# Optimization experiments

Measured on AMD Instinct MI355X. Metric: run time of the kernel, lower is better.

## Reference

```python
import jax, jax.numpy as jnp
import numpy as np

NUM_ENTITIES = 102400
NUM_RELATIONS = 1000
EMB_DIM = 256
BATCH = 512
CHUNK = 1024  # entity-table tile size; keeps the [B, CHUNK, D] diff block ~512MB


def _xavier_row_normalized(key, shape):
    # nn.init.xavier_uniform_ followed by F.normalize(p=2, dim=1)
    bound = float(np.sqrt(6.0 / (shape[0] + shape[1])))
    w = jax.random.uniform(key, shape, jnp.float32, -bound, bound)
    return w / jnp.linalg.norm(w, axis=1, keepdims=True)


def setup_inputs() -> dict:
    key = jax.random.key(0)
    k1, k2, k3, k4 = jax.random.split(key, 4)
    entity_emb = _xavier_row_normalized(k1, (NUM_ENTITIES, EMB_DIM))
    relation_emb = _xavier_row_normalized(k2, (NUM_RELATIONS, EMB_DIM))
    h_idx = jax.random.randint(k3, (BATCH,), 0, NUM_ENTITIES, dtype=jnp.int32)
    r_idx = jax.random.randint(k4, (BATCH,), 0, NUM_RELATIONS, dtype=jnp.int32)
    return {"entity_emb": entity_emb, "relation_emb": relation_emb,
            "h_idx": h_idx, "r_idx": r_idx}


def _l1_cdist(x, table, chunk=CHUNK):
    # Tiled L1 pairwise distance: avoids materializing [B, N, D].
    B, D = x.shape
    nb = table.shape[0] // chunk
    blocks = table.reshape(nb, chunk, D)

    def body(tb):  # tb: [chunk, D] -> [B, chunk]
        return jnp.sum(jnp.abs(x[:, None, :] - tb[None, :, :]), axis=-1)

    d = jax.lax.map(body, blocks)                 # [nb, B, chunk]
    return jnp.transpose(d, (1, 0, 2)).reshape(B, nb * chunk)


def reference(entity_emb, relation_emb, h_idx, r_idx):
    # TransE.score_all_tails: -cdist(h + r, all_entities, p=1)
    x = entity_emb[h_idx] + relation_emb[r_idx]   # [B, D]
    return -_l1_cdist(x, entity_emb)              # [B, NUM_ENTITIES]
```

## Files before the change

kernel.cpp:

```cpp
#include <hip/hip_runtime.h>
#include <stdint.h>

#define NE 102400
#define DIM 256
#define NB 512
#define KROW (DIM / 4)

#define BM 256
#define BN 128
#define DT 128
#define KT (DT / 4)

#define SQ 384.0f
#define NINV (-1.0f / 384.0f)

#define XQ_BYTES ((size_t)NB * KROW * 4)
#define EQ_BYTES ((size_t)NE * KROW * 4)

typedef float vf4 __attribute__((ext_vector_type(4)));

static __device__ __forceinline__ uint32_t quant4(float a, float b, float c,
                                                  float d) {
  uint32_t q = 0;
  asm("v_cvt_pk_u8_f32 %0, %1, 0, %0" : "+v"(q) : "v"(fmaf(a, SQ, 128.5f)));
  asm("v_cvt_pk_u8_f32 %0, %1, 1, %0" : "+v"(q) : "v"(fmaf(b, SQ, 128.5f)));
  asm("v_cvt_pk_u8_f32 %0, %1, 2, %0" : "+v"(q) : "v"(fmaf(c, SQ, 128.5f)));
  asm("v_cvt_pk_u8_f32 %0, %1, 3, %0" : "+v"(q) : "v"(fmaf(d, SQ, 128.5f)));
  return q;
}

__global__ __launch_bounds__(64) void make_xq_kernel(
    const float* __restrict__ ent, const float* __restrict__ rel,
    const int* __restrict__ h_idx, const int* __restrict__ r_idx,
    uint32_t* __restrict__ xq) {
  const int b = blockIdx.x;
  const int t = threadIdx.x;
  const float4 e = *(const float4*)&ent[(size_t)h_idx[b] * DIM + t * 4];
  const float4 r = *(const float4*)&rel[(size_t)r_idx[b] * DIM + t * 4];
  xq[(size_t)b * KROW + t] = quant4(e.x + r.x, e.y + r.y, e.z + r.z, e.w + r.w);
}

__global__ __launch_bounds__(256) void quant_ent_kernel(
    const float* __restrict__ ent, uint32_t* __restrict__ eq) {
  const int n = blockIdx.x * 4 + (threadIdx.x >> 6);
  const int t = threadIdx.x & 63;
  const float4 v = *(const float4*)&ent[(size_t)n * DIM + t * 4];
  eq[(size_t)n * KROW + t] = quant4(v.x, v.y, v.z, v.w);
}

__global__ __launch_bounds__(256, 2) void transe_sad_q_kernel(
    const uint32_t* __restrict__ eq, const uint32_t* __restrict__ xq,
    float* __restrict__ out) {
  __shared__ uint32_t xT[KT][BM];
  __shared__ uint32_t eT[KT][BN];

  const int n0 = blockIdx.x * BN;
  const int b0 = blockIdx.y * BM;
  const int tid = threadIdx.x;
  const int tx = tid & 15;
  const int ty = tid >> 4;
  const int s_row = tid >> 1;
  const int s_half = tid & 1;

  uint32_t acc[16][8];
#pragma unroll
  for (int i = 0; i < 16; ++i)
#pragma unroll
    for (int j = 0; j < 8; ++j) acc[i][j] = 0u;

  for (int d0 = 0; d0 < DIM; d0 += DT) {
    {
      const uint4* src = (const uint4*)&xq[(size_t)(b0 + tid) * KROW + d0 / 4];
#pragma unroll
      for (int q = 0; q < 8; ++q) {
        uint4 v = src[q];
        xT[q * 4 + 0][tid] = v.x;
        xT[q * 4 + 1][tid] = v.y;
        xT[q * 4 + 2][tid] = v.z;
        xT[q * 4 + 3][tid] = v.w;
      }
    }
    {
      const uint4* src =
          (const uint4*)&eq[(size_t)(n0 + s_row) * KROW + d0 / 4 + s_half * 16];
#pragma unroll
      for (int q = 0; q < 4; ++q) {
        uint4 v = src[q];
        const int k = s_half * 16 + q * 4;
        eT[k + 0][s_row] = v.x;
        eT[k + 1][s_row] = v.y;
        eT[k + 2][s_row] = v.z;
        eT[k + 3][s_row] = v.w;
      }
    }
    __syncthreads();

#pragma unroll 2
    for (int k = 0; k < KT; ++k) {
      uint32_t xw[16], ew[8];
      *(uint4*)&xw[0]  = *(const uint4*)&xT[k][ty * 4];
      *(uint4*)&xw[4]  = *(const uint4*)&xT[k][64 + ty * 4];
      *(uint4*)&xw[8]  = *(const uint4*)&xT[k][128 + ty * 4];
      *(uint4*)&xw[12] = *(const uint4*)&xT[k][192 + ty * 4];
      *(uint4*)&ew[0]  = *(const uint4*)&eT[k][tx * 4];
      *(uint4*)&ew[4]  = *(const uint4*)&eT[k][64 + tx * 4];
#pragma unroll
      for (int i = 0; i < 16; ++i)
#pragma unroll
        for (int j = 0; j < 8; ++j)
          asm("v_sad_u8 %0, %1, %2, %0"
              : "+v"(acc[i][j])
              : "v"(xw[i]), "v"(ew[j]));
    }
    __syncthreads();
  }

#pragma unroll
  for (int i = 0; i < 16; ++i) {
    const int b = b0 + (i >> 2) * 64 + ty * 4 + (i & 3);
    float* dst = &out[(size_t)b * NE + n0];
    vf4 o0, o1;
    o0.x = (float)acc[i][0] * NINV;
    o0.y = (float)acc[i][1] * NINV;
    o0.z = (float)acc[i][2] * NINV;
    o0.w = (float)acc[i][3] * NINV;
    o1.x = (float)acc[i][4] * NINV;
    o1.y = (float)acc[i][5] * NINV;
    o1.z = (float)acc[i][6] * NINV;
    o1.w = (float)acc[i][7] * NINV;
    __builtin_nontemporal_store(o0, (vf4*)&dst[tx * 4]);
    __builtin_nontemporal_store(o1, (vf4*)&dst[64 + tx * 4]);
  }
}

__global__ __launch_bounds__(256) void transe_sad_f32_kernel(
    const float* __restrict__ ent, const uint32_t* __restrict__ xq,
    float* __restrict__ out) {
  __shared__ uint32_t xT[KT][128];
  __shared__ uint32_t eT[KT][BN];

  const int n0 = blockIdx.x * BN;
  const int b0 = blockIdx.y * 128;
  const int tid = threadIdx.x;
  const int tx = tid & 15;
  const int ty = tid >> 4;
  const int s_row = tid >> 1;
  const int s_half = tid & 1;

  uint32_t acc[8][8];
#pragma unroll
  for (int i = 0; i < 8; ++i)
#pragma unroll
    for (int j = 0; j < 8; ++j) acc[i][j] = 0u;

  for (int d0 = 0; d0 < DIM; d0 += DT) {
    {
      const uint4* src =
          (const uint4*)&xq[(size_t)(b0 + s_row) * KROW + d0 / 4 + s_half * 16];
#pragma unroll
      for (int q = 0; q < 4; ++q) {
        uint4 v = src[q];
        const int k = s_half * 16 + q * 4;
        xT[k + 0][s_row] = v.x;
        xT[k + 1][s_row] = v.y;
        xT[k + 2][s_row] = v.z;
        xT[k + 3][s_row] = v.w;
      }
    }
    {
      const float4* src =
          (const float4*)&ent[(size_t)(n0 + s_row) * DIM + d0 + s_half * 64];
#pragma unroll
      for (int q = 0; q < 16; ++q) {
        float4 v = src[q];
        eT[s_half * 16 + q][s_row] = quant4(v.x, v.y, v.z, v.w);
      }
    }
    __syncthreads();

#pragma unroll 2
    for (int k = 0; k < KT; ++k) {
      uint32_t xw[8], ew[8];
      *(uint4*)&xw[0] = *(const uint4*)&xT[k][ty * 4];
      *(uint4*)&xw[4] = *(const uint4*)&xT[k][64 + ty * 4];
      *(uint4*)&ew[0] = *(const uint4*)&eT[k][tx * 4];
      *(uint4*)&ew[4] = *(const uint4*)&eT[k][64 + tx * 4];
#pragma unroll
      for (int i = 0; i < 8; ++i)
#pragma unroll
        for (int j = 0; j < 8; ++j)
          asm("v_sad_u8 %0, %1, %2, %0"
              : "+v"(acc[i][j])
              : "v"(xw[i]), "v"(ew[j]));
    }
    __syncthreads();
  }

#pragma unroll
  for (int i = 0; i < 8; ++i) {
    const int b = b0 + ((i & 4) << 4) + ty * 4 + (i & 3);
    float* dst = &out[(size_t)b * NE + n0];
    vf4 o0, o1;
    o0.x = (float)acc[i][0] * NINV;
    o0.y = (float)acc[i][1] * NINV;
    o0.z = (float)acc[i][2] * NINV;
    o0.w = (float)acc[i][3] * NINV;
    o1.x = (float)acc[i][4] * NINV;
    o1.y = (float)acc[i][5] * NINV;
    o1.z = (float)acc[i][6] * NINV;
    o1.w = (float)acc[i][7] * NINV;
    __builtin_nontemporal_store(o0, (vf4*)&dst[tx * 4]);
    __builtin_nontemporal_store(o1, (vf4*)&dst[64 + tx * 4]);
  }
}

extern "C" void kernel_launch(void* const* d_in, const int* in_sizes, int n_in,
                              void* d_out, int out_size, void* d_ws,
                              size_t ws_size, hipStream_t stream) {
  const float* ent = (const float*)d_in[0];
  const float* rel = (const float*)d_in[1];
  const int* h_idx = (const int*)d_in[2];
  const int* r_idx = (const int*)d_in[3];
  float* out = (float*)d_out;

  uint32_t* xq = (uint32_t*)d_ws;
  uint32_t* eq = (uint32_t*)((char*)d_ws + XQ_BYTES);

  make_xq_kernel<<<NB, 64, 0, stream>>>(ent, rel, h_idx, r_idx, xq);

  if (ws_size >= XQ_BYTES + EQ_BYTES) {
    quant_ent_kernel<<<NE / 4, 256, 0, stream>>>(ent, eq);
    dim3 grid(NE / BN, NB / BM);
    transe_sad_q_kernel<<<grid, 256, 0, stream>>>(eq, xq, out);
  } else {
    dim3 grid(NE / BN, NB / 128);
    transe_sad_f32_kernel<<<grid, 256, 0, stream>>>(ent, xq, out);
  }
}
```

Baseline: 144.0 us.

## Pre-transpose quantized operands so SAD kernel loads tiles with direct vector copies

The quantization kernels now write the query and entity codes in k-major, tile-blocked layouts. The main kernel can then fill its shared-memory tiles with contiguous 16-byte copies instead of scalar transposing stores. This removes LDS bank conflicts and per-element scatter work from the inner loop prologue. The inline-asm SAD is also swapped for the compiler builtin where it exists, which lets the compiler schedule it. The trade-off is less coalesced global writes in the quantize kernels.

```diff
diff --git a/kernel.cpp b/kernel.cpp
--- a/kernel.cpp
+++ b/kernel.cpp
@@ -5,6 +5,7 @@
 #define DIM 256
 #define NB 512
 #define KROW (DIM / 4)
+#define NTILE (NE / 128)
 
 #define BM 256
 #define BN 128
@@ -18,6 +19,16 @@
 #define EQ_BYTES ((size_t)NE * KROW * 4)
 
 typedef float vf4 __attribute__((ext_vector_type(4)));
+
+#if __has_builtin(__builtin_amdgcn_sad_u8)
+#define SAD(a, b, c) __builtin_amdgcn_sad_u8((a), (b), (c))
+#else
+static __device__ __forceinline__ uint32_t SAD(uint32_t a, uint32_t b,
+                                               uint32_t c) {
+  asm("v_sad_u8 %0, %1, %2, %0" : "+v"(c) : "v"(a), "v"(b));
+  return c;
+}
+#endif
 
 static __device__ __forceinline__ uint32_t quant4(float a, float b, float c,
                                                   float d) {
@@ -29,38 +40,43 @@
   return q;
 }
 
-__global__ __launch_bounds__(64) void make_xq_kernel(
+
+__global__ __launch_bounds__(64) void make_xqT_kernel(
     const float* __restrict__ ent, const float* __restrict__ rel,
     const int* __restrict__ h_idx, const int* __restrict__ r_idx,
-    uint32_t* __restrict__ xq) {
+    uint32_t* __restrict__ xqT) {
   const int b = blockIdx.x;
   const int t = threadIdx.x;
   const float4 e = *(const float4*)&ent[(size_t)h_idx[b] * DIM + t * 4];
   const float4 r = *(const float4*)&rel[(size_t)r_idx[b] * DIM + t * 4];
-  xq[(size_t)b * KROW + t] = quant4(e.x + r.x, e.y + r.y, e.z + r.z, e.w + r.w);
-}
-
-__global__ __launch_bounds__(256) void quant_ent_kernel(
-    const float* __restrict__ ent, uint32_t* __restrict__ eq) {
-  const int n = blockIdx.x * 4 + (threadIdx.x >> 6);
-  const int t = threadIdx.x & 63;
-  const float4 v = *(const float4*)&ent[(size_t)n * DIM + t * 4];
-  eq[(size_t)n * KROW + t] = quant4(v.x, v.y, v.z, v.w);
-}
-
-__global__ __launch_bounds__(256, 2) void transe_sad_q_kernel(
-    const uint32_t* __restrict__ eq, const uint32_t* __restrict__ xq,
+  xqT[(size_t)t * NB + b] = quant4(e.x + r.x, e.y + r.y, e.z + r.z, e.w + r.w);
+}
+
+__global__ __launch_bounds__(256) void quant_entT_kernel(
+    const float* __restrict__ ent, uint32_t* __restrict__ eqT) {
+  const int t0 = blockIdx.x;
+  const int r = threadIdx.x >> 1;
+  const int h = threadIdx.x & 1;
+  const float* src = &ent[((size_t)t0 * 128 + r) * DIM + h * 128];
+  uint32_t* dst = &eqT[(size_t)t0 * (KROW * 128) + (size_t)h * 32 * 128 + r];
+#pragma unroll
+  for (int q = 0; q < 32; ++q) {
+    const float4 v = *(const float4*)&src[q * 4];
+    dst[q * 128] = quant4(v.x, v.y, v.z, v.w);
+  }
+}
+
+__global__ __launch_bounds__(256, 2) void transe_sad_qT_kernel(
+    const uint32_t* __restrict__ eqT, const uint32_t* __restrict__ xqT,
     float* __restrict__ out) {
-  __shared__ uint32_t xT[KT][BM];
-  __shared__ uint32_t eT[KT][BN];
+  __shared__ __align__(16) uint32_t xT[KT][BM];
+  __shared__ __align__(16) uint32_t eT[KT][BN];
 
   const int n0 = blockIdx.x * BN;
   const int b0 = blockIdx.y * BM;
   const int tid = threadIdx.x;
   const int tx = tid & 15;
   const int ty = tid >> 4;
-  const int s_row = tid >> 1;
-  const int s_half = tid & 1;
 
   uint32_t acc[16][8];
 #pragma unroll
@@ -68,29 +84,24 @@
 #pragma unroll
     for (int j = 0; j < 8; ++j) acc[i][j] = 0u;
 
-  for (int d0 = 0; d0 < DIM; d0 += DT) {
-    {
-      const uint4* src = (const uint4*)&xq[(size_t)(b0 + tid) * KROW + d0 / 4];
-#pragma unroll
-      for (int q = 0; q < 8; ++q) {
-        uint4 v = src[q];
-        xT[q * 4 + 0][tid] = v.x;
-        xT[q * 4 + 1][tid] = v.y;
-        xT[q * 4 + 2][tid] = v.z;
-        xT[q * 4 + 3][tid] = v.w;
-      }
-    }
-    {
-      const uint4* src =
-          (const uint4*)&eq[(size_t)(n0 + s_row) * KROW + d0 / 4 + s_half * 16];
-#pragma unroll
-      for (int q = 0; q < 4; ++q) {
-        uint4 v = src[q];
-        const int k = s_half * 16 + q * 4;
-        eT[k + 0][s_row] = v.x;
-        eT[k + 1][s_row] = v.y;
-        eT[k + 2][s_row] = v.z;
-        eT[k + 3][s_row] = v.w;
+  for (int kb = 0; kb < KROW; kb += KT) {
+    {
+      const uint32_t* xsrc = xqT + (size_t)kb * NB + b0;
+#pragma unroll
+      for (int p = 0; p < 8; ++p) {
+        const int f = (p * 256 + tid) * 4;
+        const int k = f >> 8;
+        const int c = f & 255;
+        *(uint4*)&xT[k][c] = *(const uint4*)&xsrc[k * NB + c];
+      }
+    }
+    {
+      const uint32_t* esrc =
+          eqT + (size_t)blockIdx.x * (KROW * 128) + (size_t)kb * 128;
+#pragma unroll
+      for (int p = 0; p < 4; ++p) {
+        const int u = p * 256 + tid;
+        ((uint4*)eT)[u] = ((const uint4*)esrc)[u];
       }
     }
     __syncthreads();
@@ -107,10 +118,7 @@
 #pragma unroll
       for (int i = 0; i < 16; ++i)
 #pragma unroll
-        for (int j = 0; j < 8; ++j)
-          asm("v_sad_u8 %0, %1, %2, %0"
-              : "+v"(acc[i][j])
-              : "v"(xw[i]), "v"(ew[j]));
+        for (int j = 0; j < 8; ++j) acc[i][j] = SAD(xw[i], ew[j], acc[i][j]);
     }
     __syncthreads();
   }
@@ -133,6 +141,18 @@
   }
 }
 
+
+__global__ __launch_bounds__(64) void make_xq_kernel(
+    const float* __restrict__ ent, const float* __restrict__ rel,
+    const int* __restrict__ h_idx, const int* __restrict__ r_idx,
+    uint32_t* __restrict__ xq) {
+  const int b = blockIdx.x;
+  const int t = threadIdx.x;
+  const float4 e = *(const float4*)&ent[(size_t)h_idx[b] * DIM + t * 4];
+  const float4 r = *(const float4*)&rel[(size_t)r_idx[b] * DIM + t * 4];
+  xq[(size_t)b * KROW + t] = quant4(e.x + r.x, e.y + r.y, e.z + r.z, e.w + r.w);
+}
+
 __global__ __launch_bounds__(256) void transe_sad_f32_kernel(
     const float* __restrict__ ent, const uint32_t* __restrict__ xq,
     float* __restrict__ out) {
@@ -188,10 +208,7 @@
 #pragma unroll
       for (int i = 0; i < 8; ++i)
 #pragma unroll
-        for (int j = 0; j < 8; ++j)
-          asm("v_sad_u8 %0, %1, %2, %0"
-              : "+v"(acc[i][j])
-              : "v"(xw[i]), "v"(ew[j]));
+        for (int j = 0; j < 8; ++j) acc[i][j] = SAD(xw[i], ew[j], acc[i][j]);
     }
     __syncthreads();
   }
@@ -226,13 +243,13 @@
   uint32_t* xq = (uint32_t*)d_ws;
   uint32_t* eq = (uint32_t*)((char*)d_ws + XQ_BYTES);
 
-  make_xq_kernel<<<NB, 64, 0, stream>>>(ent, rel, h_idx, r_idx, xq);
-
   if (ws_size >= XQ_BYTES + EQ_BYTES) {
-    quant_ent_kernel<<<NE / 4, 256, 0, stream>>>(ent, eq);
+    make_xqT_kernel<<<NB, 64, 0, stream>>>(ent, rel, h_idx, r_idx, xq);
+    quant_entT_kernel<<<NTILE, 256, 0, stream>>>(ent, eq);
     dim3 grid(NE / BN, NB / BM);
-    transe_sad_q_kernel<<<grid, 256, 0, stream>>>(eq, xq, out);
+    transe_sad_qT_kernel<<<grid, 256, 0, stream>>>(eq, xq, out);
   } else {
+    make_xq_kernel<<<NB, 64, 0, stream>>>(ent, rel, h_idx, r_idx, xq);
     dim3 grid(NE / BN, NB / 128);
     transe_sad_f32_kernel<<<grid, 256, 0, stream>>>(ent, xq, out);
   }
```

New measurement: 167.9 us. 16.6% more time.
